# Kernel optimization log

Hardware: AMD Instinct MI355X
Metric: run time of the kernel (lower is better)

The kernel has to match this reference:

```python
import jax, jax.numpy as jnp
import numpy as np

ROUTINGS = 3
NUM_CAPSULE = 32
DIM_CAPSULE = 64
K_EPSILON = 1e-7  # keras K.epsilon()


def squash(x, axis=-1):
    s = jnp.sum(jnp.square(x), axis=axis, keepdims=True) + K_EPSILON
    scale = jnp.sqrt(s) / (0.5 + s)
    return scale * x


def setup_inputs() -> dict:
    key = jax.random.key(0)
    k1, k2 = jax.random.split(key)
    B, N_in, D_in = 32, 1024, 512
    u = jax.random.normal(k1, (B, N_in, D_in), dtype=jnp.float32)
    # glorot_uniform for capsule_kernel (conv1d width-1 kernel == dense matrix)
    fan_out = NUM_CAPSULE * DIM_CAPSULE
    limit = float(np.sqrt(6.0 / (D_in + fan_out)))
    W = jax.random.uniform(k2, (D_in, fan_out), jnp.float32, -limit, limit)
    return {"u": u, "W": W}


def reference(u, W):
    B, N_in, _ = u.shape
    # K.conv1d with width-1 kernel == matmul, then reshape
    u_hat = (u @ W).reshape(B, N_in, NUM_CAPSULE, DIM_CAPSULE)
    u_hat = jnp.transpose(u_hat, (0, 2, 1, 3))  # [B, N_out, N_in, D]
    b = jnp.zeros(u_hat.shape[:3], u_hat.dtype)  # [B, N_out, N_in]
    vj = None
    for i in range(ROUTINGS):
        Wv = jax.nn.softmax(b, axis=1)  # softmax over output capsules (axis=1)
        vj = jnp.einsum('bon,bond->bod', Wv, u_hat)  # batch_dot(Wv,u_hat,[2,2])
        if i < ROUTINGS - 1:
            # K.l2_normalize(vj) with default axis=None -> global L2 norm
            norm = jnp.sqrt(jnp.maximum(jnp.sum(jnp.square(vj)), 1e-12))
            vjn = vj / norm
            b = jnp.einsum('bod,bond->bon', vjn, u_hat)  # batch_dot(vj,u_hat,[2,3])
    return squash(vj)
```

## Files before the change

### kernel.cpp

```cpp
#include <hip/hip_runtime.h>
#include <hip/hip_bf16.h>


constexpr int B = 32, N = 1024, K = 512, O = 32, D = 64, F = 2048;
constexpr int NT = 32;
constexpr int ST = 72;

typedef __attribute__((ext_vector_type(8))) short bf16x8;
typedef __attribute__((ext_vector_type(4))) float f32x4;

__device__ inline unsigned int pk_hi(float x, float y) {
  union { __hip_bfloat162 h; unsigned int u; } c;
  c.h = __float22bfloat162_rn(float2{x, y});
  return c.u;
}
__device__ inline unsigned short bf16_1(float x) {
  return (unsigned short)(pk_hi(x, 0.f) & 0xffffu);
}
__device__ inline void split2(float x, unsigned short& h, unsigned short& l) {
  h = bf16_1(x);
  l = bf16_1(x - __uint_as_float((unsigned int)h << 16));
}
__device__ inline float bf2f(unsigned short h) {
  return __uint_as_float((unsigned int)h << 16);
}
__device__ inline int swz(int r) { return ((r >> 3) & 7) << 3; }

__device__ inline void stage_hi(unsigned short* hi, int r, int c4, float4 v) {
  int c = c4 ^ swz(r);
  uint2 p;
  p.x = pk_hi(v.x, v.y);
  p.y = pk_hi(v.z, v.w);
  *(uint2*)&hi[r * ST + c] = p;
}
__device__ inline void stage_hilo(unsigned short* hi, unsigned short* lo, int r,
                                  int c4, float4 v) {
  int c = c4 ^ swz(r);
  uint2 ph, pl;
  ph.x = pk_hi(v.x, v.y);
  ph.y = pk_hi(v.z, v.w);
  pl.x = pk_hi(v.x - __uint_as_float(ph.x << 16),
               v.y - __uint_as_float(ph.x & 0xffff0000u));
  pl.y = pk_hi(v.z - __uint_as_float(ph.y << 16),
               v.w - __uint_as_float(ph.y & 0xffff0000u));
  *(uint2*)&hi[r * ST + c] = ph;
  *(uint2*)&lo[r * ST + c] = pl;
}
__device__ inline bf16x8 frag_row(const unsigned short* p, int r, int k0) {
  return *(const bf16x8*)&p[r * ST + (k0 ^ swz(r))];
}
__device__ inline bf16x8 frag_col(const unsigned short* p, int c, int n0) {
  bf16x8 f;
#pragma unroll
  for (int j = 0; j < 8; j++) {
    int n = n0 + j;
    f[j] = (short)p[n * ST + (c ^ swz(n))];
  }
  return f;
}

__global__ __launch_bounds__(256) void k_colsum(const float* __restrict__ u,
                                                float* __restrict__ cs) {
  int b = blockIdx.x, n0 = blockIdx.y * 32;
  int kq = (threadIdx.x & 127) * 4, ng = threadIdx.x >> 7;
  const float* ub = u + ((size_t)b * N + n0 + ng * 16) * K + kq;
  float4 a = {0.f, 0.f, 0.f, 0.f};
#pragma unroll
  for (int r = 0; r < 16; r++) {
    float4 v = *(const float4*)&ub[(size_t)r * K];
    a.x += v.x; a.y += v.y; a.z += v.z; a.w += v.w;
  }
  __shared__ float4 red[128];
  if (ng) red[threadIdx.x & 127] = a;
  __syncthreads();
  if (!ng) {
    float4 o = red[threadIdx.x];
    atomicAdd(&cs[b * K + kq + 0], (a.x + o.x) * (1.f / 32.f));
    atomicAdd(&cs[b * K + kq + 1], (a.y + o.y) * (1.f / 32.f));
    atomicAdd(&cs[b * K + kq + 2], (a.z + o.z) * (1.f / 32.f));
    atomicAdd(&cs[b * K + kq + 3], (a.w + o.w) * (1.f / 32.f));
  }
}

__global__ __launch_bounds__(512) void k_vjt(const unsigned short* __restrict__ Sp,
                                             const float* __restrict__ colsum,
                                             const float* __restrict__ W,
                                             float* __restrict__ sumsq, int slot,
                                             float* __restrict__ t) {
  __shared__ __align__(16) float s_s[K];
  __shared__ float red[7][D];
  __shared__ __align__(16) float vs[D];
  int bo = blockIdx.x, b = bo >> 5, o = bo & 31;
  int d = threadIdx.x & 63, ks = threadIdx.x >> 6;
  if (slot == 0) {
    for (int i = threadIdx.x; i < K; i += 512) s_s[i] = colsum[(size_t)b * K + i];
  } else {
    const unsigned short* base = Sp + ((size_t)b * NT * O + o) * K;
    int i = threadIdx.x;
    float a = 0.f;
#pragma unroll
    for (int nt = 0; nt < NT; nt++) a += bf2f(base[(size_t)nt * O * K + i]);
    s_s[i] = a;
  }
  __syncthreads();
  float acc = 0.f;
  const float* Wc = W + (size_t)o * D + d;
  for (int k = ks * 64; k < ks * 64 + 64; k += 4) {
    acc += s_s[k] * Wc[(size_t)k * F] + s_s[k + 1] * Wc[(size_t)(k + 1) * F] +
           s_s[k + 2] * Wc[(size_t)(k + 2) * F] + s_s[k + 3] * Wc[(size_t)(k + 3) * F];
  }
  if (ks) red[ks - 1][d] = acc;
  __syncthreads();
  if (ks == 0) {
#pragma unroll
    for (int j = 0; j < 7; j++) acc += red[j][d];
    vs[d] = acc;
    float ss = acc * acc;
#pragma unroll
    for (int m = 32; m >= 1; m >>= 1) ss += __shfl_xor(ss, m, 64);
    if (d == 0) atomicAdd(&sumsq[slot], ss);
  }
  __syncthreads();
  {
    int wave = threadIdx.x >> 6, lane = threadIdx.x & 63;
    int rr = lane >> 3, dc = lane & 7;
    float4 va = *(const float4*)&vs[dc * 8];
    float4 vb = *(const float4*)&vs[dc * 8 + 4];
#pragma unroll
    for (int i = 0; i < 8; i++) {
      int kk = wave * 64 + i * 8 + rr;
      const float* Wr = W + (size_t)kk * F + o * 64 + dc * 8;
      float4 wa = *(const float4*)Wr;
      float4 wb = *(const float4*)(Wr + 4);
      float p = wa.x * va.x + wa.y * va.y + wa.z * va.z + wa.w * va.w +
                wb.x * vb.x + wb.y * vb.y + wb.z * vb.z + wb.w * vb.w;
      p += __shfl_xor(p, 1, 64);
      p += __shfl_xor(p, 2, 64);
      p += __shfl_xor(p, 4, 64);
      if (dc == 0) t[(size_t)bo * K + kk] = p;
    }
  }
}

__global__ __launch_bounds__(512) void k_out(const unsigned short* __restrict__ Sp,
                                             const float* __restrict__ W,
                                             float* __restrict__ out) {
  __shared__ __align__(16) float s_s[K];
  __shared__ float red[7][D];
  int bo = blockIdx.x, b = bo >> 5, o = bo & 31;
  int d = threadIdx.x & 63, ks = threadIdx.x >> 6;
  {
    const unsigned short* base = Sp + ((size_t)b * NT * O + o) * K;
    int i = threadIdx.x;
    float a = 0.f;
#pragma unroll
    for (int nt = 0; nt < NT; nt++) a += bf2f(base[(size_t)nt * O * K + i]);
    s_s[i] = a;
  }
  __syncthreads();
  float acc = 0.f;
  const float* Wc = W + (size_t)o * D + d;
  for (int k = ks * 64; k < ks * 64 + 64; k += 4) {
    acc += s_s[k] * Wc[(size_t)k * F] + s_s[k + 1] * Wc[(size_t)(k + 1) * F] +
           s_s[k + 2] * Wc[(size_t)(k + 2) * F] + s_s[k + 3] * Wc[(size_t)(k + 3) * F];
  }
  if (ks) red[ks - 1][d] = acc;
  __syncthreads();
  if (ks == 0) {
#pragma unroll
    for (int j = 0; j < 7; j++) acc += red[j][d];
    float ss = acc * acc;
#pragma unroll
    for (int m = 32; m >= 1; m >>= 1) ss += __shfl_xor(ss, m, 64);
    float s = ss + 1e-7f;
    out[(size_t)bo * D + d] = (sqrtf(s) / (0.5f + s)) * acc;
  }
}

__global__ __launch_bounds__(256, 4) void k_route(const float* __restrict__ t,
                                                  const float* __restrict__ u,
                                                  const float* __restrict__ sumsq,
                                                  int slot,
                                                  unsigned short* __restrict__ Sp) {
  __shared__ unsigned short u_hi[32 * ST];
  __shared__ unsigned short t_hi[32 * ST], t_lo[32 * ST];
  __shared__ float wv[32 * 36];
  __shared__ float psum[8 * 36];
  __shared__ float mbuf[36];
  unsigned short* wvh = t_hi;
  unsigned short* wvl = t_lo;

  const int b = blockIdx.x, n0 = blockIdx.y * 32;
  const int tid = threadIdx.x, lane = tid & 63, wave = tid >> 6;
  const int m = lane & 15, oct = lane >> 4;
  const float* ub = u + ((size_t)b * N + n0) * K;
  const float* tb = t + (size_t)b * O * K;
  const float nrm_inv = rsqrtf(fmaxf(sumsq[slot], 1e-12f));

  const int mo = wave & 1, nt = wave >> 1;
  f32x4 accb = {0.f, 0.f, 0.f, 0.f};
  for (int kc = 0; kc < K; kc += 64) {
    __syncthreads();
#pragma unroll
    for (int h = 0; h < 2; h++) {
      int i = tid + h * 256;
      int r = i >> 4, c4 = (i & 15) * 4;
      stage_hilo(t_hi, t_lo, r, c4, *(const float4*)&tb[(size_t)r * K + kc + c4]);
      stage_hi(u_hi, r, c4, *(const float4*)&ub[(size_t)r * K + kc + c4]);
    }
    __syncthreads();
#pragma unroll
    for (int ks = 0; ks < 64; ks += 32) {
      bf16x8 ah = frag_row(t_hi, mo * 16 + m, ks + oct * 8);
      bf16x8 al = frag_row(t_lo, mo * 16 + m, ks + oct * 8);
      bf16x8 bh = frag_row(u_hi, nt * 16 + m, ks + oct * 8);
      accb = __builtin_amdgcn_mfma_f32_16x16x32_bf16(ah, bh, accb, 0, 0, 0);
      accb = __builtin_amdgcn_mfma_f32_16x16x32_bf16(al, bh, accb, 0, 0, 0);
    }
  }
  __syncthreads();
#pragma unroll
  for (int r = 0; r < 4; r++)
    wv[(mo * 16 + oct * 4 + r) * 36 + nt * 16 + m] = accb[r] * nrm_inv;
  __syncthreads();

  {
    int n = tid & 31, g = tid >> 5;
    float m4 = -1e30f;
#pragma unroll
    for (int j = 0; j < 4; j++) m4 = fmaxf(m4, wv[(g * 4 + j) * 36 + n]);
    psum[g * 36 + n] = m4;
    __syncthreads();
    if (tid < 32) {
      float mx = psum[tid];
#pragma unroll
      for (int gg = 1; gg < 8; gg++) mx = fmaxf(mx, psum[gg * 36 + tid]);
      mbuf[tid] = mx;
    }
    __syncthreads();
    float mx = mbuf[n];
    float s4 = 0.f;
#pragma unroll
    for (int j = 0; j < 4; j++) {
      float e = __expf(wv[(g * 4 + j) * 36 + n] - mx);
      wv[(g * 4 + j) * 36 + n] = e;
      s4 += e;
    }
    psum[g * 36 + n] = s4;
    __syncthreads();
    if (tid < 32) {
      float s = 0.f;
#pragma unroll
      for (int gg = 0; gg < 8; gg++) s += psum[gg * 36 + tid];
      mbuf[tid] = 1.f / s;
    }
    __syncthreads();
    float inv = mbuf[n];
#pragma unroll
    for (int j = 0; j < 4; j++) {
      unsigned short h, l;
      split2(wv[(g * 4 + j) * 36 + n] * inv, h, l);
      wvh[(g * 4 + j) * ST + n] = h;
      wvl[(g * 4 + j) * ST + n] = l;
    }
  }
  __syncthreads();

  const int mo2 = wave & 1, kp = wave >> 1;
  const int o0 = mo2 * 16;
  bf16x8 a_h = *(const bf16x8*)&wvh[(o0 + m) * ST + oct * 8];
  bf16x8 a_l = *(const bf16x8*)&wvl[(o0 + m) * ST + oct * 8];
  unsigned short* Sb = Sp + ((size_t)b * NT + blockIdx.y) * O * K;
  for (int kc = 0; kc < K; kc += 64) {
    __syncthreads();
#pragma unroll
    for (int h = 0; h < 2; h++) {
      int i = tid + h * 256;
      int r = i >> 4, c4 = (i & 15) * 4;
      stage_hi(u_hi, r, c4, *(const float4*)&ub[(size_t)r * K + kc + c4]);
    }
    __syncthreads();
#pragma unroll
    for (int kt = kp * 2; kt < kp * 2 + 2; kt++) {
      int c = kt * 16 + m;
      bf16x8 bh = frag_col(u_hi, c, oct * 8);
      f32x4 acs = {0.f, 0.f, 0.f, 0.f};
      acs = __builtin_amdgcn_mfma_f32_16x16x32_bf16(a_h, bh, acs, 0, 0, 0);
      acs = __builtin_amdgcn_mfma_f32_16x16x32_bf16(a_l, bh, acs, 0, 0, 0);
#pragma unroll
      for (int r = 0; r < 4; r++)
        Sb[(size_t)(o0 + oct * 4 + r) * K + kc + c] = bf16_1(acs[r]);
    }
  }
}

extern "C" void kernel_launch(void* const* d_in, const int* in_sizes, int n_in,
                              void* d_out, int out_size, void* d_ws, size_t ws_size,
                              hipStream_t stream) {
  const float* u = (const float*)d_in[0];
  const float* W = (const float*)d_in[1];
  float* out = (float*)d_out;

  char* ws = (char*)d_ws;
  unsigned short* Sp = (unsigned short*)ws;
  float* t = (float*)(Sp + (size_t)B * NT * O * K);
  float* colsum = t + (size_t)B * O * K;
  float* sumsq = colsum + (size_t)B * K;

  hipMemsetAsync(colsum, 0, ((size_t)B * K + 16) * sizeof(float), stream);

  k_colsum<<<dim3(B, 32), 256, 0, stream>>>(u, colsum);
  k_vjt<<<B * O, 512, 0, stream>>>(Sp, colsum, W, sumsq, 0, t);
  k_route<<<dim3(B, NT), 256, 0, stream>>>(t, u, sumsq, 0, Sp);
  k_vjt<<<B * O, 512, 0, stream>>>(Sp, colsum, W, sumsq, 1, t);
  k_route<<<dim3(B, NT), 256, 0, stream>>>(t, u, sumsq, 1, Sp);
  k_out<<<B * O, 512, 0, stream>>>(Sp, W, out);
}
```

Baseline: 201.5 us.

## Pre-convert u and t to bf16 once and replace atomics with partial buffers

The prep kernel now writes a bf16 copy of u alongside the column sums. Each k_route pass then streams half the bytes, with no per-chunk conversion. k_vjt stores t already split into hi/lo bf16. The colsum and sum-of-squares atomics, and the memset they needed, become per-block partial buffers that the consumers reduce. This adds a 32 MB bf16 write of u and a redundant partial-sum reduction in every route block, in exchange for about halving u traffic in the four route loops.

```diff
diff --git a/kernel.cpp b/kernel.cpp
--- a/kernel.cpp
+++ b/kernel.cpp
@@ -26,26 +26,6 @@
 }
 __device__ inline int swz(int r) { return ((r >> 3) & 7) << 3; }
 
-__device__ inline void stage_hi(unsigned short* hi, int r, int c4, float4 v) {
-  int c = c4 ^ swz(r);
-  uint2 p;
-  p.x = pk_hi(v.x, v.y);
-  p.y = pk_hi(v.z, v.w);
-  *(uint2*)&hi[r * ST + c] = p;
-}
-__device__ inline void stage_hilo(unsigned short* hi, unsigned short* lo, int r,
-                                  int c4, float4 v) {
-  int c = c4 ^ swz(r);
-  uint2 ph, pl;
-  ph.x = pk_hi(v.x, v.y);
-  ph.y = pk_hi(v.z, v.w);
-  pl.x = pk_hi(v.x - __uint_as_float(ph.x << 16),
-               v.y - __uint_as_float(ph.x & 0xffff0000u));
-  pl.y = pk_hi(v.z - __uint_as_float(ph.y << 16),
-               v.w - __uint_as_float(ph.y & 0xffff0000u));
-  *(uint2*)&hi[r * ST + c] = ph;
-  *(uint2*)&lo[r * ST + c] = pl;
-}
 __device__ inline bf16x8 frag_row(const unsigned short* p, int r, int k0) {
   return *(const bf16x8*)&p[r * ST + (k0 ^ swz(r))];
 }
@@ -59,47 +39,60 @@
   return f;
 }
 
-__global__ __launch_bounds__(256) void k_colsum(const float* __restrict__ u,
-                                                float* __restrict__ cs) {
-  int b = blockIdx.x, n0 = blockIdx.y * 32;
-  int kq = (threadIdx.x & 127) * 4, ng = threadIdx.x >> 7;
+__global__ __launch_bounds__(256) void k_prep(const float* __restrict__ u,
+                                              float* __restrict__ cs_part,
+                                              unsigned short* __restrict__ u_bf) {
+  __shared__ float4 red[128];
+  int b = blockIdx.x, ntile = blockIdx.y, n0 = ntile * 32;
+  int tid = threadIdx.x;
+  int kq = (tid & 127) * 4, ng = tid >> 7;
   const float* ub = u + ((size_t)b * N + n0 + ng * 16) * K + kq;
+  unsigned short* ubf = u_bf + ((size_t)b * N + n0 + ng * 16) * K + kq;
   float4 a = {0.f, 0.f, 0.f, 0.f};
 #pragma unroll
-  for (int r = 0; r < 16; r++) {
-    float4 v = *(const float4*)&ub[(size_t)r * K];
+  for (int nn = 0; nn < 16; nn++) {
+    float4 v = *(const float4*)&ub[(size_t)nn * K];
     a.x += v.x; a.y += v.y; a.z += v.z; a.w += v.w;
-  }
-  __shared__ float4 red[128];
-  if (ng) red[threadIdx.x & 127] = a;
+    uint2 p;
+    p.x = pk_hi(v.x, v.y);
+    p.y = pk_hi(v.z, v.w);
+    *(uint2*)&ubf[(size_t)nn * K] = p;
+  }
+  if (ng) red[tid & 127] = a;
   __syncthreads();
   if (!ng) {
-    float4 o = red[threadIdx.x];
-    atomicAdd(&cs[b * K + kq + 0], (a.x + o.x) * (1.f / 32.f));
-    atomicAdd(&cs[b * K + kq + 1], (a.y + o.y) * (1.f / 32.f));
-    atomicAdd(&cs[b * K + kq + 2], (a.z + o.z) * (1.f / 32.f));
-    atomicAdd(&cs[b * K + kq + 3], (a.w + o.w) * (1.f / 32.f));
+    float4 o = red[tid];
+    float* cs = cs_part + ((size_t)b * 32 + ntile) * K + kq;
+    cs[0] = (a.x + o.x) * (1.f / 32.f);
+    cs[1] = (a.y + o.y) * (1.f / 32.f);
+    cs[2] = (a.z + o.z) * (1.f / 32.f);
+    cs[3] = (a.w + o.w) * (1.f / 32.f);
   }
 }
 
 __global__ __launch_bounds__(512) void k_vjt(const unsigned short* __restrict__ Sp,
-                                             const float* __restrict__ colsum,
+                                             const float* __restrict__ cs_part,
                                              const float* __restrict__ W,
-                                             float* __restrict__ sumsq, int slot,
-                                             float* __restrict__ t) {
+                                             float* __restrict__ ssq_part, int slot,
+                                             unsigned short* __restrict__ t_hi,
+                                             unsigned short* __restrict__ t_lo) {
   __shared__ __align__(16) float s_s[K];
   __shared__ float red[7][D];
   __shared__ __align__(16) float vs[D];
   int bo = blockIdx.x, b = bo >> 5, o = bo & 31;
   int d = threadIdx.x & 63, ks = threadIdx.x >> 6;
-  if (slot == 0) {
-    for (int i = threadIdx.x; i < K; i += 512) s_s[i] = colsum[(size_t)b * K + i];
-  } else {
-    const unsigned short* base = Sp + ((size_t)b * NT * O + o) * K;
+  {
     int i = threadIdx.x;
     float a = 0.f;
-#pragma unroll
-    for (int nt = 0; nt < NT; nt++) a += bf2f(base[(size_t)nt * O * K + i]);
+    if (slot == 0) {
+      const float* base = cs_part + (size_t)b * 32 * K;
+#pragma unroll
+      for (int nt = 0; nt < 32; nt++) a += base[(size_t)nt * K + i];
+    } else {
+      const unsigned short* base = Sp + ((size_t)b * NT * O + o) * K;
+#pragma unroll
+      for (int nt = 0; nt < NT; nt++) a += bf2f(base[(size_t)nt * O * K + i]);
+    }
     s_s[i] = a;
   }
   __syncthreads();
@@ -118,7 +111,7 @@
     float ss = acc * acc;
 #pragma unroll
     for (int m = 32; m >= 1; m >>= 1) ss += __shfl_xor(ss, m, 64);
-    if (d == 0) atomicAdd(&sumsq[slot], ss);
+    if (d == 0) ssq_part[slot * 1024 + bo] = ss;
   }
   __syncthreads();
   {
@@ -137,7 +130,12 @@
       p += __shfl_xor(p, 1, 64);
       p += __shfl_xor(p, 2, 64);
       p += __shfl_xor(p, 4, 64);
-      if (dc == 0) t[(size_t)bo * K + kk] = p;
+      if (dc == 0) {
+        unsigned short h, l;
+        split2(p, h, l);
+        t_hi[(size_t)bo * K + kk] = h;
+        t_lo[(size_t)bo * K + kk] = l;
+      }
     }
   }
 }
@@ -177,9 +175,10 @@
   }
 }
 
-__global__ __launch_bounds__(256, 4) void k_route(const float* __restrict__ t,
-                                                  const float* __restrict__ u,
-                                                  const float* __restrict__ sumsq,
+__global__ __launch_bounds__(256, 4) void k_route(const unsigned short* __restrict__ t_hi_g,
+                                                  const unsigned short* __restrict__ t_lo_g,
+                                                  const unsigned short* __restrict__ u_bf,
+                                                  const float* __restrict__ ssq_part,
                                                   int slot,
                                                   unsigned short* __restrict__ Sp) {
   __shared__ unsigned short u_hi[32 * ST];
@@ -193,20 +192,25 @@
   const int b = blockIdx.x, n0 = blockIdx.y * 32;
   const int tid = threadIdx.x, lane = tid & 63, wave = tid >> 6;
   const int m = lane & 15, oct = lane >> 4;
-  const float* ub = u + ((size_t)b * N + n0) * K;
-  const float* tb = t + (size_t)b * O * K;
-  const float nrm_inv = rsqrtf(fmaxf(sumsq[slot], 1e-12f));
+  const unsigned short* ubf = u_bf + ((size_t)b * N + n0) * K;
+  const unsigned short* thg = t_hi_g + (size_t)b * O * K;
+  const unsigned short* tlg = t_lo_g + (size_t)b * O * K;
+
+  const int sr = tid >> 3, sc8 = (tid & 7) * 8;
+  const int scs = sc8 ^ swz(sr);
 
   const int mo = wave & 1, nt = wave >> 1;
   f32x4 accb = {0.f, 0.f, 0.f, 0.f};
   for (int kc = 0; kc < K; kc += 64) {
     __syncthreads();
-#pragma unroll
-    for (int h = 0; h < 2; h++) {
-      int i = tid + h * 256;
-      int r = i >> 4, c4 = (i & 15) * 4;
-      stage_hilo(t_hi, t_lo, r, c4, *(const float4*)&tb[(size_t)r * K + kc + c4]);
-      stage_hi(u_hi, r, c4, *(const float4*)&ub[(size_t)r * K + kc + c4]);
+    {
+      const size_t go = (size_t)sr * K + kc;
+      *(uint4*)&t_hi[sr * ST + scs] = *(const uint4*)&thg[go + sc8];
+      *(uint4*)&t_hi[sr * ST + (scs ^ 8) ] = *(const uint4*)&thg[go + (sc8 ^ 8)];
+      *(uint4*)&t_lo[sr * ST + scs] = *(const uint4*)&tlg[go + sc8];
+      *(uint4*)&t_lo[sr * ST + (scs ^ 8)] = *(const uint4*)&tlg[go + (sc8 ^ 8)];
+      *(uint4*)&u_hi[sr * ST + scs] = *(const uint4*)&ubf[go + sc8];
+      *(uint4*)&u_hi[sr * ST + (scs ^ 8)] = *(const uint4*)&ubf[go + (sc8 ^ 8)];
     }
     __syncthreads();
 #pragma unroll
@@ -219,6 +223,23 @@
     }
   }
   __syncthreads();
+  {
+    const float* sp = ssq_part + slot * 1024;
+    float sa = 0.f;
+#pragma unroll
+    for (int j = 0; j < 4; j++) sa += sp[tid + j * 256];
+    psum[tid & 255] = sa;
+    __syncthreads();
+    if (tid < 64) {
+      float s = psum[tid] + psum[tid + 64] + psum[tid + 128] + psum[tid + 192];
+#pragma unroll
+      for (int mm = 32; mm >= 1; mm >>= 1) s += __shfl_xor(s, mm, 64);
+      if (tid == 0) mbuf[0] = rsqrtf(fmaxf(s, 1e-12f));
+    }
+    __syncthreads();
+  }
+  const float nrm_inv = mbuf[0];
+  __syncthreads();
 #pragma unroll
   for (int r = 0; r < 4; r++)
     wv[(mo * 16 + oct * 4 + r) * 36 + nt * 16 + m] = accb[r] * nrm_inv;
@@ -273,11 +294,10 @@
   unsigned short* Sb = Sp + ((size_t)b * NT + blockIdx.y) * O * K;
   for (int kc = 0; kc < K; kc += 64) {
     __syncthreads();
-#pragma unroll
-    for (int h = 0; h < 2; h++) {
-      int i = tid + h * 256;
-      int r = i >> 4, c4 = (i & 15) * 4;
-      stage_hi(u_hi, r, c4, *(const float4*)&ub[(size_t)r * K + kc + c4]);
+    {
+      const size_t go = (size_t)sr * K + kc;
+      *(uint4*)&u_hi[sr * ST + scs] = *(const uint4*)&ubf[go + sc8];
+      *(uint4*)&u_hi[sr * ST + (scs ^ 8)] = *(const uint4*)&ubf[go + (sc8 ^ 8)];
     }
     __syncthreads();
 #pragma unroll
@@ -303,16 +323,16 @@
 
   char* ws = (char*)d_ws;
   unsigned short* Sp = (unsigned short*)ws;
-  float* t = (float*)(Sp + (size_t)B * NT * O * K);
-  float* colsum = t + (size_t)B * O * K;
-  float* sumsq = colsum + (size_t)B * K;
-
-  hipMemsetAsync(colsum, 0, ((size_t)B * K + 16) * sizeof(float), stream);
-
-  k_colsum<<<dim3(B, 32), 256, 0, stream>>>(u, colsum);
-  k_vjt<<<B * O, 512, 0, stream>>>(Sp, colsum, W, sumsq, 0, t);
-  k_route<<<dim3(B, NT), 256, 0, stream>>>(t, u, sumsq, 0, Sp);
-  k_vjt<<<B * O, 512, 0, stream>>>(Sp, colsum, W, sumsq, 1, t);
-  k_route<<<dim3(B, NT), 256, 0, stream>>>(t, u, sumsq, 1, Sp);
+  unsigned short* u_bf = Sp + (size_t)B * NT * O * K;
+  unsigned short* t_hi = u_bf + (size_t)B * N * K;
+  unsigned short* t_lo = t_hi + (size_t)B * O * K;
+  float* cs_part = (float*)(t_lo + (size_t)B * O * K);
+  float* ssq_part = cs_part + (size_t)B * 32 * K;
+
+  k_prep<<<dim3(B, 32), 256, 0, stream>>>(u, cs_part, u_bf);
+  k_vjt<<<B * O, 512, 0, stream>>>(Sp, cs_part, W, ssq_part, 0, t_hi, t_lo);
+  k_route<<<dim3(B, NT), 256, 0, stream>>>(t_hi, t_lo, u_bf, ssq_part, 0, Sp);
+  k_vjt<<<B * O, 512, 0, stream>>>(Sp, cs_part, W, ssq_part, 1, t_hi, t_lo);
+  k_route<<<dim3(B, NT), 256, 0, stream>>>(t_hi, t_lo, u_bf, ssq_part, 1, Sp);
   k_out<<<B * O, 512, 0, stream>>>(Sp, W, out);
 }
```

New measurement: 190.3 us. 1.06x faster.
